# Kernel optimization log

Hardware: AMD Instinct MI355X
Metric: run time of the kernel (lower is better)

## Reference

```python
import jax, jax.numpy as jnp
import numpy as np

DECAY = 0.999
EPS = 1e-05
COMMIT = 0.25


def _layer_norm(x, g, b, eps=1e-5):
    mu = x.mean(-1, keepdims=True)
    var = ((x - mu) ** 2).mean(-1, keepdims=True)
    return (x - mu) * jax.lax.rsqrt(var + eps) * g + b


def setup_inputs() -> dict:
    key = jax.random.key(0)
    ks = jax.random.split(key, 8)
    B, T, D, M, H = 8, 4096, 512, 1024, 512
    init_bound = 1.0 / 512
    embedding = jax.random.uniform(ks[0], (M, D), jnp.float32, -init_bound, init_bound)
    return {
        "dense_x": jax.random.normal(ks[1], (B, T, D), jnp.float32),
        "dense_padding_mask": jax.random.randint(ks[2], (B, T), 0, 2).astype(bool),
        "labels": jax.random.randint(ks[3], (B, T), 0, M),
        "embedding": embedding,
        "ema_count": jnp.zeros((M,), jnp.float32),
        "ema_weight": embedding,
        "ln1_g": jnp.ones((D,), jnp.float32),
        "ln1_b": jnp.zeros((D,), jnp.float32),
        "W1": jax.random.normal(ks[4], (D, H), jnp.float32) * (1.0 / np.sqrt(D)),
        "ln2_g": jnp.ones((H,), jnp.float32),
        "ln2_b": jnp.zeros((H,), jnp.float32),
        "W2": jax.random.normal(ks[5], (H, M), jnp.float32) * (1.0 / np.sqrt(H)),
    }


def reference(dense_x, dense_padding_mask, labels, embedding, ema_count, ema_weight,
              ln1_g, ln1_b, W1, ln2_g, ln2_b, W2):
    B, T, D = dense_x.shape
    M = embedding.shape[0]
    N = B * T

    # ---- VQ codebook (EMA) ----
    x_flat = jax.lax.stop_gradient(dense_x).reshape(N, D)
    distances = (jnp.sum(embedding ** 2, axis=1)[None, :]
                 + jnp.sum(x_flat ** 2, axis=1, keepdims=True)
                 - 2.0 * (x_flat @ embedding.T))
    indices = jnp.argmin(distances, axis=-1)  # [N]
    quantized = embedding[indices].reshape(B, T, D)

    # EMA codebook update (training path); encodings.sum(0) and encodings.T @ x
    # expressed as scatter-adds instead of materializing [N, M] one-hot.
    counts = jnp.zeros((M,), dense_x.dtype).at[indices].add(1.0)
    new_count = DECAY * ema_count + (1.0 - DECAY) * counts
    n = jnp.sum(new_count)
    new_count = (new_count + EPS) / (n + M * EPS) * n
    dw = jnp.zeros((M, D), dense_x.dtype).at[indices].add(x_flat)
    new_weight = DECAY * ema_weight + (1.0 - DECAY) * dw
    new_embedding = new_weight / new_count[:, None]

    e_latent_loss = (dense_x - jax.lax.stop_gradient(quantized)) ** 2  # [B,T,D]
    vq_loss = COMMIT * e_latent_loss
    quantized_st = dense_x + jax.lax.stop_gradient(quantized - dense_x)

    avg_probs = counts / N
    perplexity = jnp.exp(-jnp.sum(avg_probs * jnp.log(avg_probs + 1e-10)))

    # ---- decoder: LN -> ReLU -> Linear -> LN -> ReLU -> Linear ----
    h = jax.nn.relu(_layer_norm(dense_x, ln1_g, ln1_b)) @ W1      # [B,T,H]
    logits = jax.nn.relu(_layer_norm(h, ln2_g, ln2_b)) @ W2       # [B,T,M]

    # ---- cross-entropy with ignore_index=-1 (padding) ----
    lab = jnp.where(dense_padding_mask, -1, labels)
    valid = lab >= 0
    safe = jnp.where(valid, lab, 0)
    logp = jax.nn.log_softmax(logits, axis=-1)
    ce = -jnp.take_along_axis(logp, safe[..., None], axis=-1)[..., 0]
    recon_loss = jnp.where(valid, ce, 0.0)

    loss = recon_loss + vq_loss.sum(-1)  # [B,T]
    return quantized_st, loss, perplexity, new_embedding, new_count, new_weight
```

## Files before the change

### kernel.cpp

```cpp
#include <hip/hip_runtime.h>


#define N_TOK 32768

typedef __attribute__((ext_vector_type(8))) short short8;
typedef __attribute__((ext_vector_type(4))) float f32x4;

__device__ __forceinline__ f32x4 mfma16(short8 a, short8 b, f32x4 c) {
    return __builtin_amdgcn_mfma_f32_16x16x32_bf16(a, b, c, 0, 0, 0);
}

__device__ __forceinline__ void gl_lds16(const void* g, void* l) {
    __builtin_amdgcn_global_load_lds(
        (const __attribute__((address_space(1))) void*)g,
        (__attribute__((address_space(3))) void*)l, 16, 0, 0);
}

__device__ __forceinline__ unsigned short f2bf(float x) {
    unsigned u = __float_as_uint(x);
    u += 0x7fffu + ((u >> 16) & 1u);
    return (unsigned short)(u >> 16);
}
__device__ __forceinline__ float bf2f(unsigned short h) {
    return __uint_as_float(((unsigned)h) << 16);
}

__device__ __forceinline__ float waveSum(float v) {
#pragma unroll
    for (int off = 32; off > 0; off >>= 1) v += __shfl_down(v, off, 64);
    return v;
}
__device__ __forceinline__ float xorSum(float v) {
#pragma unroll
    for (int off = 1; off < 64; off <<= 1) v += __shfl_xor(v, off);
    return v;
}

__device__ __forceinline__ void stage_tile128(const unsigned short* __restrict__ src,
                                              int r0, int k0, short* lds,
                                              int w, int lane) {
#pragma unroll
    for (int iss = 0; iss < 2; ++iss) {
        int L = (w << 11) + (iss << 10) + (lane << 4);
        int kb = L >> 11, m = (L >> 4) & 127;
        gl_lds16(src + (((size_t)(r0 + m)) << 9) + k0 + (kb << 3), (char*)lds + L);
    }
}

__global__ __launch_bounds__(256) void prep_x_kernel(
        const float* __restrict__ X, const float* __restrict__ g,
        const float* __restrict__ b, unsigned short* __restrict__ Xh,
        unsigned short* __restrict__ Xl, unsigned short* __restrict__ A1) {
    int lane = threadIdx.x & 63;
    int n = (blockIdx.x << 2) + (threadIdx.x >> 6);
    const float* row = X + ((size_t)n << 9);
    float v[8]; float s = 0.f, ss = 0.f;
#pragma unroll
    for (int i = 0; i < 8; ++i) { v[i] = row[lane + (i << 6)]; s += v[i]; ss += v[i] * v[i]; }
    s = xorSum(s); ss = xorSum(ss);
    float mu = s * (1.f / 512.f);
    float rs = rsqrtf(ss * (1.f / 512.f) - mu * mu + 1e-5f);
#pragma unroll
    for (int i = 0; i < 8; ++i) {
        int c = lane + (i << 6);
        size_t o = ((size_t)n << 9) + c;
        float x = v[i];
        unsigned short h = f2bf(x);
        Xh[o] = h;
        Xl[o] = f2bf(x - bf2f(h));
        float a = fmaxf((x - mu) * rs * g[c] + b[c], 0.f);
        A1[o] = f2bf(a);
    }
}

__global__ __launch_bounds__(256) void prep_h_kernel(
        const unsigned short* __restrict__ Hb, const float* __restrict__ g,
        const float* __restrict__ b, unsigned short* __restrict__ A2) {
    int lane = threadIdx.x & 63;
    int n = (blockIdx.x << 2) + (threadIdx.x >> 6);
    const unsigned short* row = Hb + ((size_t)n << 9);
    float v[8]; float s = 0.f, ss = 0.f;
#pragma unroll
    for (int i = 0; i < 8; ++i) { v[i] = bf2f(row[lane + (i << 6)]); s += v[i]; ss += v[i] * v[i]; }
    s = xorSum(s); ss = xorSum(ss);
    float mu = s * (1.f / 512.f);
    float rs = rsqrtf(ss * (1.f / 512.f) - mu * mu + 1e-5f);
#pragma unroll
    for (int i = 0; i < 8; ++i) {
        int c = lane + (i << 6);
        float a = fmaxf((v[i] - mu) * rs * g[c] + b[c], 0.f);
        A2[((size_t)n << 9) + c] = f2bf(a);
    }
}

__global__ __launch_bounds__(256) void prep_e_kernel(
        const float* __restrict__ E, unsigned short* __restrict__ Eh,
        unsigned short* __restrict__ El, float* __restrict__ e_sq) {
    int lane = threadIdx.x & 63;
    int m = (blockIdx.x << 2) + (threadIdx.x >> 6);
    const float* row = E + ((size_t)m << 9);
    float ss = 0.f;
#pragma unroll
    for (int i = 0; i < 8; ++i) {
        int c = lane + (i << 6);
        float x = row[c];
        ss += x * x;
        unsigned short h = f2bf(x);
        size_t o = ((size_t)m << 9) + c;
        Eh[o] = h;
        El[o] = f2bf(x - bf2f(h));
    }
    ss = xorSum(ss);
    if (lane == 0) e_sq[m] = ss;
}

__global__ __launch_bounds__(256) void prep_wt_kernel(
        const float* __restrict__ W, unsigned short* __restrict__ WT, int Nw) {
    __shared__ float t[32][33];
    int n0 = blockIdx.x << 5, k0 = blockIdx.y << 5;
    int tx = threadIdx.x & 31, ty = threadIdx.x >> 5;
#pragma unroll
    for (int l = 0; l < 4; ++l)
        t[ty + (l << 3)][tx] = W[(size_t)(k0 + ty + (l << 3)) * Nw + n0 + tx];
    __syncthreads();
#pragma unroll
    for (int l = 0; l < 4; ++l)
        WT[(((size_t)(n0 + ty + (l << 3))) << 9) + k0 + tx] = f2bf(t[tx][ty + (l << 3)]);
}

__device__ __forceinline__ unsigned long long packDist(float d, int m) {
    unsigned u = __float_as_uint(d);
    u = (u & 0x80000000u) ? ~u : (u | 0x80000000u);
    return ((unsigned long long)u << 32) | (unsigned)m;
}

__global__ __launch_bounds__(256) void dist_mfma_kernel(
        const unsigned short* __restrict__ Xh, const unsigned short* __restrict__ Xl,
        const unsigned short* __restrict__ Eh, const unsigned short* __restrict__ El,
        const float* __restrict__ e_sq, unsigned long long* __restrict__ minpack) {
    __shared__ __align__(16) short Ah[4096], Al[4096], Bh[4096], Bl[4096];
    int tid = threadIdx.x, lane = tid & 63, w = tid >> 6;
    int quad = lane >> 4, lanelo = lane & 15;
    int wm = w >> 1, wn = w & 1;
    int row0 = blockIdx.x << 7, m0 = blockIdx.y << 7;
    f32x4 acc[4][4];
#pragma unroll
    for (int i = 0; i < 4; ++i)
#pragma unroll
        for (int j = 0; j < 4; ++j) acc[i][j] = 0.f;

    for (int k0 = 0; k0 < 512; k0 += 32) {
        stage_tile128(Xh, row0, k0, Ah, w, lane);
        stage_tile128(Xl, row0, k0, Al, w, lane);
        stage_tile128(Eh, m0, k0, Bh, w, lane);
        stage_tile128(El, m0, k0, Bl, w, lane);
        __syncthreads();
        short8 ah[4], alr[4], bh[4], blr[4];
#pragma unroll
        for (int i = 0; i < 4; ++i) {
            int m = (wm << 6) + (i << 4) + lanelo;
            ah[i]  = *(const short8*)&Ah[(quad << 10) + (m << 3)];
            alr[i] = *(const short8*)&Al[(quad << 10) + (m << 3)];
        }
#pragma unroll
        for (int j = 0; j < 4; ++j) {
            int n = (wn << 6) + (j << 4) + lanelo;
            bh[j]  = *(const short8*)&Bh[(quad << 10) + (n << 3)];
            blr[j] = *(const short8*)&Bl[(quad << 10) + (n << 3)];
        }
#pragma unroll
        for (int i = 0; i < 4; ++i)
#pragma unroll
            for (int j = 0; j < 4; ++j) {
                acc[i][j] = mfma16(ah[i],  bh[j],  acc[i][j]);
                acc[i][j] = mfma16(alr[i], bh[j],  acc[i][j]);
                acc[i][j] = mfma16(ah[i],  blr[j], acc[i][j]);
            }
        __syncthreads();
    }

    float esq[4];
#pragma unroll
    for (int j = 0; j < 4; ++j) esq[j] = e_sq[m0 + (wn << 6) + (j << 4) + lanelo];
#pragma unroll
    for (int i = 0; i < 4; ++i)
#pragma unroll
        for (int r = 0; r < 4; ++r) {
            unsigned long long best = ~0ULL;
#pragma unroll
            for (int j = 0; j < 4; ++j) {
                int code = m0 + (wn << 6) + (j << 4) + lanelo;
                float d = esq[j] - 2.f * acc[i][j][r];
                unsigned long long p = packDist(d, code);
                if (p < best) best = p;
            }
#pragma unroll
            for (int off = 1; off < 16; off <<= 1) {
                unsigned long long q = __shfl_xor(best, off);
                if (q < best) best = q;
            }
            if (lanelo == 0) {
                int t = row0 + (wm << 6) + (i << 4) + (quad << 2) + r;
                atomicMin(&minpack[t], best);
            }
        }
}

__global__ __launch_bounds__(256) void gather_kernel(
        const float* __restrict__ X, const float* __restrict__ E,
        const unsigned long long* __restrict__ minpack,
        float* __restrict__ out_q, float* __restrict__ counts,
        float* __restrict__ vqsum) {
    int lane = threadIdx.x & 63;
    int n = (blockIdx.x << 2) + (threadIdx.x >> 6);
    int idx = (int)(minpack[n] & 0xFFFFFFFFULL);
    if (lane == 0) atomicAdd(&counts[idx], 1.0f);
    const float* xr = X + ((size_t)n << 9);
    const float* er = E + ((size_t)idx << 9);
    float s = 0.f;
#pragma unroll
    for (int i = 0; i < 8; ++i) {
        int c = lane + (i << 6);
        float xv = xr[c], q = er[c];
        out_q[((size_t)n << 9) + c] = q;
        float dlt = xv - q;
        s += dlt * dlt;
    }
    s = waveSum(s);
    if (lane == 0) vqsum[n] = 0.25f * s;
}

__global__ __launch_bounds__(256) void dw_kernel(
        const float* __restrict__ X, const unsigned long long* __restrict__ minpack,
        float* __restrict__ dw) {
    __shared__ float acc[4][512];
    int tid = threadIdx.x, lane = tid & 63, w = tid >> 6;
    int m = blockIdx.x;
    for (int c = lane; c < 512; c += 64) acc[w][c] = 0.f;
    for (int n0 = (w << 13); n0 < ((w + 1) << 13); n0 += 64) {
        int idx = (int)(minpack[n0 + lane] & 0xFFFFFFFFULL);
        unsigned long long hit = __ballot(idx == m);
        while (hit) {
            int t = __ffsll((unsigned long long)hit) - 1;
            hit &= hit - 1;
            const float* xr = X + ((size_t)(n0 + t) << 9);
#pragma unroll
            for (int i = 0; i < 8; ++i) acc[w][lane + (i << 6)] += xr[lane + (i << 6)];
        }
    }
    __syncthreads();
    for (int c = tid; c < 512; c += 256)
        dw[((size_t)m << 9) + c] = acc[0][c] + acc[1][c] + acc[2][c] + acc[3][c];
}

__global__ __launch_bounds__(256) void gemm1_mfma_kernel(
        const unsigned short* __restrict__ A1, const unsigned short* __restrict__ W1T,
        unsigned short* __restrict__ Hb) {
    __shared__ __align__(16) short As[4096], Bs[4096];
    int tid = threadIdx.x, lane = tid & 63, w = tid >> 6;
    int quad = lane >> 4, lanelo = lane & 15;
    int wm = w >> 1, wn = w & 1;
    int row0 = blockIdx.x << 7, n0 = blockIdx.y << 7;
    f32x4 acc[4][4];
#pragma unroll
    for (int i = 0; i < 4; ++i)
#pragma unroll
        for (int j = 0; j < 4; ++j) acc[i][j] = 0.f;

    for (int k0 = 0; k0 < 512; k0 += 32) {
        stage_tile128(A1, row0, k0, As, w, lane);
        stage_tile128(W1T, n0, k0, Bs, w, lane);
        __syncthreads();
        short8 af[4], bf[4];
#pragma unroll
        for (int i = 0; i < 4; ++i) {
            int m = (wm << 6) + (i << 4) + lanelo;
            af[i] = *(const short8*)&As[(quad << 10) + (m << 3)];
        }
#pragma unroll
        for (int j = 0; j < 4; ++j) {
            int n = (wn << 6) + (j << 4) + lanelo;
            bf[j] = *(const short8*)&Bs[(quad << 10) + (n << 3)];
        }
#pragma unroll
        for (int i = 0; i < 4; ++i)
#pragma unroll
            for (int j = 0; j < 4; ++j) acc[i][j] = mfma16(af[i], bf[j], acc[i][j]);
        __syncthreads();
    }
#pragma unroll
    for (int i = 0; i < 4; ++i)
#pragma unroll
        for (int j = 0; j < 4; ++j)
#pragma unroll
            for (int r = 0; r < 4; ++r) {
                int row = row0 + (wm << 6) + (i << 4) + (quad << 2) + r;
                int col = n0 + (wn << 6) + (j << 4) + lanelo;
                Hb[((size_t)row << 9) + col] = f2bf(acc[i][j][r]);
            }
}

__global__ __launch_bounds__(256) void gemm2_chunk_kernel(
        const unsigned short* __restrict__ A2, const unsigned short* __restrict__ W2T,
        const int* __restrict__ mask, const int* __restrict__ labels,
        float* __restrict__ ws_cmax, float* __restrict__ ws_csum,
        float* __restrict__ ws_lab) {
    __shared__ __align__(16) short As[4096], Bs[4096];
    __shared__ float lmax[2][2][64], lsum[2][2][64], llab[128];
    __shared__ int slab[128];
    int tid = threadIdx.x, lane = tid & 63, w = tid >> 6;
    int quad = lane >> 4, lanelo = lane & 15;
    int wm = w >> 1, wn = w & 1;
    int row0 = blockIdx.x << 7, c0 = blockIdx.y << 7;
    if (tid < 128) {
        int mk = mask[row0 + tid];
        slab[tid] = mk ? 0 : labels[row0 + tid];
    }
    f32x4 acc[4][4];
#pragma unroll
    for (int i = 0; i < 4; ++i)
#pragma unroll
        for (int j = 0; j < 4; ++j) acc[i][j] = 0.f;

    for (int k0 = 0; k0 < 512; k0 += 32) {
        stage_tile128(A2, row0, k0, As, w, lane);
        stage_tile128(W2T, c0, k0, Bs, w, lane);
        __syncthreads();
        short8 af[4], bf[4];
#pragma unroll
        for (int i = 0; i < 4; ++i) {
            int m = (wm << 6) + (i << 4) + lanelo;
            af[i] = *(const short8*)&As[(quad << 10) + (m << 3)];
        }
#pragma unroll
        for (int j = 0; j < 4; ++j) {
            int n = (wn << 6) + (j << 4) + lanelo;
            bf[j] = *(const short8*)&Bs[(quad << 10) + (n << 3)];
        }
#pragma unroll
        for (int i = 0; i < 4; ++i)
#pragma unroll
            for (int j = 0; j < 4; ++j) acc[i][j] = mfma16(af[i], bf[j], acc[i][j]);
        __syncthreads();
    }

#pragma unroll
    for (int i = 0; i < 4; ++i)
#pragma unroll
        for (int j = 0; j < 4; ++j)
#pragma unroll
            for (int r = 0; r < 4; ++r) {
                int code = c0 + (wn << 6) + (j << 4) + lanelo;
                int tt = (wm << 6) + (i << 4) + (quad << 2) + r;
                if (code == slab[tt]) llab[tt] = acc[i][j][r];
            }
#pragma unroll
    for (int i = 0; i < 4; ++i)
#pragma unroll
        for (int r = 0; r < 4; ++r) {
            float mx = fmaxf(fmaxf(acc[i][0][r], acc[i][1][r]),
                             fmaxf(acc[i][2][r], acc[i][3][r]));
#pragma unroll
            for (int off = 1; off < 16; off <<= 1) mx = fmaxf(mx, __shfl_xor(mx, off));
            if (lanelo == 0) lmax[wm][wn][(i << 4) + (quad << 2) + r] = mx;
        }
    __syncthreads();
#pragma unroll
    for (int i = 0; i < 4; ++i)
#pragma unroll
        for (int r = 0; r < 4; ++r) {
            int tl = (i << 4) + (quad << 2) + r;
            float cm = fmaxf(lmax[wm][0][tl], lmax[wm][1][tl]);
            float s = expf(acc[i][0][r] - cm) + expf(acc[i][1][r] - cm) +
                      expf(acc[i][2][r] - cm) + expf(acc[i][3][r] - cm);
#pragma unroll
            for (int off = 1; off < 16; off <<= 1) s += __shfl_xor(s, off);
            if (lanelo == 0) lsum[wm][wn][tl] = s;
        }
    __syncthreads();
    if (tid < 128) {
        int wmi = tid >> 6, tl = tid & 63;
        int token = row0 + tid;
        float cm = fmaxf(lmax[wmi][0][tl], lmax[wmi][1][tl]);
        float cs = lsum[wmi][0][tl] + lsum[wmi][1][tl];
        size_t o = ((size_t)blockIdx.y << 15) + token;
        ws_cmax[o] = cm;
        ws_csum[o] = cs;
        if ((slab[tid] >> 7) == (int)blockIdx.y) ws_lab[token] = llab[tid];
    }
}

__global__ __launch_bounds__(256) void ce_combine_kernel(
        const float* __restrict__ ws_cmax, const float* __restrict__ ws_csum,
        const float* __restrict__ ws_lab, const int* __restrict__ mask,
        const float* __restrict__ vqsum, float* __restrict__ loss_out) {
    int n = (blockIdx.x << 8) + threadIdx.x;
    float m[8], s[8];
#pragma unroll
    for (int c = 0; c < 8; ++c) {
        m[c] = ws_cmax[(c << 15) + n];
        s[c] = ws_csum[(c << 15) + n];
    }
    float gm = m[0];
#pragma unroll
    for (int c = 1; c < 8; ++c) gm = fmaxf(gm, m[c]);
    float se = 0.f;
#pragma unroll
    for (int c = 0; c < 8; ++c) se += s[c] * expf(m[c] - gm);
    float ce = -(ws_lab[n] - gm - logf(se));
    loss_out[n] = (mask[n] ? 0.f : ce) + vqsum[n];
}

__global__ __launch_bounds__(1024) void codebook_kernel(
        const float* __restrict__ ema_count, const float* __restrict__ counts,
        float* __restrict__ out_perp, float* __restrict__ out_newcount) {
    __shared__ float red[16];
    int tid = threadIdx.x;
    int lane = tid & 63, wid = tid >> 6;
    float cnt = counts[tid];
    float raw = 0.999f * ema_count[tid] + 0.001f * cnt;
    float v = waveSum(raw);
    if (lane == 0) red[wid] = v;
    __syncthreads();
    float nsum = 0.f;
#pragma unroll
    for (int i = 0; i < 16; ++i) nsum += red[i];
    __syncthreads();
    float p = cnt * (1.f / 32768.f);
    float e = p * logf(p + 1e-10f);
    e = waveSum(e);
    if (lane == 0) red[wid] = e;
    __syncthreads();
    float ent = 0.f;
#pragma unroll
    for (int i = 0; i < 16; ++i) ent += red[i];
    float nc = (raw + 1e-5f) / (nsum + 1024.f * 1e-5f) * nsum;
    out_newcount[tid] = nc;
    if (tid == 0) out_perp[0] = expf(-ent);
}

__global__ __launch_bounds__(256) void newweight_kernel(
        const float* __restrict__ ema_weight, const float* __restrict__ dw,
        const float* __restrict__ newcount, float* __restrict__ out_neww,
        float* __restrict__ out_newemb) {
    int i = (blockIdx.x << 8) + threadIdx.x;
    float nw = 0.999f * ema_weight[i] + 0.001f * dw[i];
    out_neww[i] = nw;
    out_newemb[i] = nw / newcount[i >> 9];
}

extern "C" void kernel_launch(void* const* d_in, const int* in_sizes, int n_in,
                              void* d_out, int out_size, void* d_ws, size_t ws_size,
                              hipStream_t stream) {
    const float* X          = (const float*)d_in[0];
    const int*   mask       = (const int*)d_in[1];
    const int*   labels     = (const int*)d_in[2];
    const float* E          = (const float*)d_in[3];
    const float* ema_count  = (const float*)d_in[4];
    const float* ema_weight = (const float*)d_in[5];
    const float* g1 = (const float*)d_in[6];
    const float* b1 = (const float*)d_in[7];
    const float* W1 = (const float*)d_in[8];
    const float* g2 = (const float*)d_in[9];
    const float* b2 = (const float*)d_in[10];
    const float* W2 = (const float*)d_in[11];

    float* out = (float*)d_out;
    float* out_q        = out;
    float* out_loss     = out + 16777216;
    float* out_perp     = out + 16809984;
    float* out_newemb   = out + 16809985;
    float* out_newcount = out + 17334273;
    float* out_neww     = out + 17335297;

    float* w = (float*)d_ws;
    float* vqsum = w;  w += 32768;
    float* e_sq = w;   w += 1024;
    float* counts = w; w += 1024;
    float* dwbuf = w;  w += 524288;
    unsigned long long* minpack = (unsigned long long*)w; w += 65536;
    float* ws_cmax = w; w += 262144;
    float* ws_csum = w; w += 262144;
    float* ws_lab  = w; w += 32768;
    unsigned short* Eh  = (unsigned short*)w; w += 262144;
    unsigned short* El  = (unsigned short*)w; w += 262144;
    unsigned short* W1T = (unsigned short*)w; w += 131072;
    unsigned short* W2T = (unsigned short*)w; w += 262144;
    unsigned short* Xh  = (unsigned short*)w; w += 8388608;
    unsigned short* Xl  = (unsigned short*)w; w += 8388608;
    unsigned short* A1  = (unsigned short*)w; w += 8388608;
    unsigned short* A2  = Xh;
    unsigned short* Hb  = Xl;

    hipMemsetAsync(counts, 0, 1024 * sizeof(float), stream);
    hipMemsetAsync(minpack, 0xFF, (size_t)N_TOK * sizeof(unsigned long long), stream);

    prep_e_kernel<<<256, 256, 0, stream>>>(E, Eh, El, e_sq);
    prep_wt_kernel<<<dim3(16, 16), 256, 0, stream>>>(W1, W1T, 512);
    prep_wt_kernel<<<dim3(32, 16), 256, 0, stream>>>(W2, W2T, 1024);
    prep_x_kernel<<<8192, 256, 0, stream>>>(X, g1, b1, Xh, Xl, A1);
    dist_mfma_kernel<<<dim3(256, 8), 256, 0, stream>>>(Xh, Xl, Eh, El, e_sq, minpack);
    gather_kernel<<<8192, 256, 0, stream>>>(X, E, minpack, out_q, counts, vqsum);
    dw_kernel<<<1024, 256, 0, stream>>>(X, minpack, dwbuf);
    gemm1_mfma_kernel<<<dim3(256, 4), 256, 0, stream>>>(A1, W1T, Hb);
    prep_h_kernel<<<8192, 256, 0, stream>>>(Hb, g2, b2, A2);
    gemm2_chunk_kernel<<<dim3(256, 8), 256, 0, stream>>>(A2, W2T, mask, labels,
                                                         ws_cmax, ws_csum, ws_lab);
    ce_combine_kernel<<<128, 256, 0, stream>>>(ws_cmax, ws_csum, ws_lab,
                                               mask, vqsum, out_loss);
    codebook_kernel<<<1, 1024, 0, stream>>>(ema_count, counts, out_perp, out_newcount);
    newweight_kernel<<<2048, 256, 0, stream>>>(ema_weight, dwbuf, out_newcount,
                                               out_neww, out_newemb);
}
```

Measured before the change: 548.5 us.

## Use fp16 two-term distance GEMM and bucket tokens by code for dw

The VQ distance GEMM drops from three bf16 MFMAs per tile (split X and split E) to two fp16 MFMAs. X is stored as a single fp16 value and the codebook is pre-scaled by 512 and split into fp16 hi/lo parts, which also removes one LDS staging buffer and one global input stream. The dw accumulation no longer has each of 1024 blocks scan all 32768 indices with ballots. Instead, integer counts feed a prefix-sum in the codebook kernel, a scatter kernel builds per-code token buckets, and dw reads only its own bucket. This adds two small kernels and an extra 16 MB workspace buffer for Hb, and a single fp16 copy of X may change argmin tie-breaking near equal distances.

```diff
diff --git a/kernel.cpp b/kernel.cpp
--- a/kernel.cpp
+++ b/kernel.cpp
@@ -4,10 +4,14 @@
 #define N_TOK 32768
 
 typedef __attribute__((ext_vector_type(8))) short short8;
+typedef _Float16 half8 __attribute__((ext_vector_type(8)));
 typedef __attribute__((ext_vector_type(4))) float f32x4;
 
 __device__ __forceinline__ f32x4 mfma16(short8 a, short8 b, f32x4 c) {
     return __builtin_amdgcn_mfma_f32_16x16x32_bf16(a, b, c, 0, 0, 0);
+}
+__device__ __forceinline__ f32x4 mfma16h(half8 a, half8 b, f32x4 c) {
+    return __builtin_amdgcn_mfma_f32_16x16x32_f16(a, b, c, 0, 0, 0);
 }
 
 __device__ __forceinline__ void gl_lds16(const void* g, void* l) {
@@ -24,6 +28,16 @@
 __device__ __forceinline__ float bf2f(unsigned short h) {
     return __uint_as_float(((unsigned)h) << 16);
 }
+__device__ __forceinline__ unsigned short f2h(float x) {
+    union { _Float16 h; unsigned short u; } c;
+    c.h = (_Float16)x;
+    return c.u;
+}
+__device__ __forceinline__ float h2f(unsigned short u) {
+    union { _Float16 h; unsigned short u; } c;
+    c.u = u;
+    return (float)c.h;
+}
 
 __device__ __forceinline__ float waveSum(float v) {
 #pragma unroll
@@ -49,8 +63,8 @@
 
 __global__ __launch_bounds__(256) void prep_x_kernel(
         const float* __restrict__ X, const float* __restrict__ g,
-        const float* __restrict__ b, unsigned short* __restrict__ Xh,
-        unsigned short* __restrict__ Xl, unsigned short* __restrict__ A1) {
+        const float* __restrict__ b, unsigned short* __restrict__ Xf,
+        unsigned short* __restrict__ A1) {
     int lane = threadIdx.x & 63;
     int n = (blockIdx.x << 2) + (threadIdx.x >> 6);
     const float* row = X + ((size_t)n << 9);
@@ -65,9 +79,7 @@
         int c = lane + (i << 6);
         size_t o = ((size_t)n << 9) + c;
         float x = v[i];
-        unsigned short h = f2bf(x);
-        Xh[o] = h;
-        Xl[o] = f2bf(x - bf2f(h));
+        Xf[o] = f2h(x);
         float a = fmaxf((x - mu) * rs * g[c] + b[c], 0.f);
         A1[o] = f2bf(a);
     }
@@ -94,8 +106,8 @@
 }
 
 __global__ __launch_bounds__(256) void prep_e_kernel(
-        const float* __restrict__ E, unsigned short* __restrict__ Eh,
-        unsigned short* __restrict__ El, float* __restrict__ e_sq) {
+        const float* __restrict__ E, unsigned short* __restrict__ Ehf,
+        unsigned short* __restrict__ Elf, float* __restrict__ e_sq) {
     int lane = threadIdx.x & 63;
     int m = (blockIdx.x << 2) + (threadIdx.x >> 6);
     const float* row = E + ((size_t)m << 9);
@@ -105,13 +117,14 @@
         int c = lane + (i << 6);
         float x = row[c];
         ss += x * x;
-        unsigned short h = f2bf(x);
+        float xs = x * 512.f;
+        unsigned short h = f2h(xs);
         size_t o = ((size_t)m << 9) + c;
-        Eh[o] = h;
-        El[o] = f2bf(x - bf2f(h));
+        Ehf[o] = h;
+        Elf[o] = f2h(xs - h2f(h));
     }
     ss = xorSum(ss);
-    if (lane == 0) e_sq[m] = ss;
+    if (lane == 0) e_sq[m] = ss * 512.f;
 }
 
 __global__ __launch_bounds__(256) void prep_wt_kernel(
@@ -135,10 +148,10 @@
 }
 
 __global__ __launch_bounds__(256) void dist_mfma_kernel(
-        const unsigned short* __restrict__ Xh, const unsigned short* __restrict__ Xl,
-        const unsigned short* __restrict__ Eh, const unsigned short* __restrict__ El,
+        const unsigned short* __restrict__ Xf,
+        const unsigned short* __restrict__ Ehf, const unsigned short* __restrict__ Elf,
         const float* __restrict__ e_sq, unsigned long long* __restrict__ minpack) {
-    __shared__ __align__(16) short Ah[4096], Al[4096], Bh[4096], Bl[4096];
+    __shared__ __align__(16) short Axs[4096], Bh[4096], Bl[4096];
     int tid = threadIdx.x, lane = tid & 63, w = tid >> 6;
     int quad = lane >> 4, lanelo = lane & 15;
     int wm = w >> 1, wn = w & 1;
@@ -150,31 +163,28 @@
         for (int j = 0; j < 4; ++j) acc[i][j] = 0.f;
 
     for (int k0 = 0; k0 < 512; k0 += 32) {
-        stage_tile128(Xh, row0, k0, Ah, w, lane);
-        stage_tile128(Xl, row0, k0, Al, w, lane);
-        stage_tile128(Eh, m0, k0, Bh, w, lane);
-        stage_tile128(El, m0, k0, Bl, w, lane);
-        __syncthreads();
-        short8 ah[4], alr[4], bh[4], blr[4];
+        stage_tile128(Xf, row0, k0, Axs, w, lane);
+        stage_tile128(Ehf, m0, k0, Bh, w, lane);
+        stage_tile128(Elf, m0, k0, Bl, w, lane);
+        __syncthreads();
+        half8 av[4], bh[4], bl[4];
 #pragma unroll
         for (int i = 0; i < 4; ++i) {
             int m = (wm << 6) + (i << 4) + lanelo;
-            ah[i]  = *(const short8*)&Ah[(quad << 10) + (m << 3)];
-            alr[i] = *(const short8*)&Al[(quad << 10) + (m << 3)];
+            av[i] = __builtin_bit_cast(half8, *(const short8*)&Axs[(quad << 10) + (m << 3)]);
         }
 #pragma unroll
         for (int j = 0; j < 4; ++j) {
             int n = (wn << 6) + (j << 4) + lanelo;
-            bh[j]  = *(const short8*)&Bh[(quad << 10) + (n << 3)];
-            blr[j] = *(const short8*)&Bl[(quad << 10) + (n << 3)];
+            bh[j] = __builtin_bit_cast(half8, *(const short8*)&Bh[(quad << 10) + (n << 3)]);
+            bl[j] = __builtin_bit_cast(half8, *(const short8*)&Bl[(quad << 10) + (n << 3)]);
         }
 #pragma unroll
         for (int i = 0; i < 4; ++i)
 #pragma unroll
             for (int j = 0; j < 4; ++j) {
-                acc[i][j] = mfma16(ah[i],  bh[j],  acc[i][j]);
-                acc[i][j] = mfma16(alr[i], bh[j],  acc[i][j]);
-                acc[i][j] = mfma16(ah[i],  blr[j], acc[i][j]);
+                acc[i][j] = mfma16h(av[i], bh[j], acc[i][j]);
+                acc[i][j] = mfma16h(av[i], bl[j], acc[i][j]);
             }
         __syncthreads();
     }
@@ -209,12 +219,12 @@
 __global__ __launch_bounds__(256) void gather_kernel(
         const float* __restrict__ X, const float* __restrict__ E,
         const unsigned long long* __restrict__ minpack,
-        float* __restrict__ out_q, float* __restrict__ counts,
+        float* __restrict__ out_q, int* __restrict__ icounts,
         float* __restrict__ vqsum) {
     int lane = threadIdx.x & 63;
     int n = (blockIdx.x << 2) + (threadIdx.x >> 6);
     int idx = (int)(minpack[n] & 0xFFFFFFFFULL);
-    if (lane == 0) atomicAdd(&counts[idx], 1.0f);
+    if (lane == 0) atomicAdd(&icounts[idx], 1);
     const float* xr = X + ((size_t)n << 9);
     const float* er = E + ((size_t)idx << 9);
     float s = 0.f;
@@ -230,27 +240,77 @@
     if (lane == 0) vqsum[n] = 0.25f * s;
 }
 
+__global__ __launch_bounds__(1024) void codebook_kernel(
+        const float* __restrict__ ema_count, const int* __restrict__ icounts,
+        float* __restrict__ out_perp, float* __restrict__ out_newcount,
+        int* __restrict__ offsets) {
+    __shared__ int sc[1024];
+    __shared__ float red[16];
+    int tid = threadIdx.x;
+    int lane = tid & 63, wid = tid >> 6;
+    int ic = icounts[tid];
+    sc[tid] = ic;
+    for (int off = 1; off < 1024; off <<= 1) {
+        __syncthreads();
+        int v = (tid >= off) ? sc[tid - off] : 0;
+        __syncthreads();
+        sc[tid] += v;
+    }
+    offsets[tid] = sc[tid] - ic;
+    __syncthreads();
+
+    float cnt = (float)ic;
+    float raw = 0.999f * ema_count[tid] + 0.001f * cnt;
+    float v = waveSum(raw);
+    if (lane == 0) red[wid] = v;
+    __syncthreads();
+    float nsum = 0.f;
+#pragma unroll
+    for (int i = 0; i < 16; ++i) nsum += red[i];
+    __syncthreads();
+    float p = cnt * (1.f / 32768.f);
+    float e = p * logf(p + 1e-10f);
+    e = waveSum(e);
+    if (lane == 0) red[wid] = e;
+    __syncthreads();
+    float ent = 0.f;
+#pragma unroll
+    for (int i = 0; i < 16; ++i) ent += red[i];
+    float nc = (raw + 1e-5f) / (nsum + 1024.f * 1e-5f) * nsum;
+    out_newcount[tid] = nc;
+    if (tid == 0) out_perp[0] = expf(-ent);
+}
+
+__global__ __launch_bounds__(256) void scatter_kernel(
+        const unsigned long long* __restrict__ minpack,
+        const int* __restrict__ offsets, int* __restrict__ cursor,
+        int* __restrict__ bucket) {
+    int n = (blockIdx.x << 8) + threadIdx.x;
+    int idx = (int)(minpack[n] & 0xFFFFFFFFULL);
+    int pos = atomicAdd(&cursor[idx], 1);
+    bucket[offsets[idx] + pos] = n;
+}
+
 __global__ __launch_bounds__(256) void dw_kernel(
-        const float* __restrict__ X, const unsigned long long* __restrict__ minpack,
+        const float* __restrict__ X, const int* __restrict__ bucket,
+        const int* __restrict__ icounts, const int* __restrict__ offsets,
         float* __restrict__ dw) {
-    __shared__ float acc[4][512];
+    __shared__ float comb[4][512];
     int tid = threadIdx.x, lane = tid & 63, w = tid >> 6;
     int m = blockIdx.x;
-    for (int c = lane; c < 512; c += 64) acc[w][c] = 0.f;
-    for (int n0 = (w << 13); n0 < ((w + 1) << 13); n0 += 64) {
-        int idx = (int)(minpack[n0 + lane] & 0xFFFFFFFFULL);
-        unsigned long long hit = __ballot(idx == m);
-        while (hit) {
-            int t = __ffsll((unsigned long long)hit) - 1;
-            hit &= hit - 1;
-            const float* xr = X + ((size_t)(n0 + t) << 9);
-#pragma unroll
-            for (int i = 0; i < 8; ++i) acc[w][lane + (i << 6)] += xr[lane + (i << 6)];
-        }
-    }
+    int cnt = icounts[m], base = offsets[m];
+    float acc[8] = {};
+    for (int i = w; i < cnt; i += 4) {
+        int t = bucket[base + i];
+        const float* xr = X + ((size_t)t << 9);
+#pragma unroll
+        for (int j = 0; j < 8; ++j) acc[j] += xr[lane + (j << 6)];
+    }
+#pragma unroll
+    for (int j = 0; j < 8; ++j) comb[w][lane + (j << 6)] = acc[j];
     __syncthreads();
     for (int c = tid; c < 512; c += 256)
-        dw[((size_t)m << 9) + c] = acc[0][c] + acc[1][c] + acc[2][c] + acc[3][c];
+        dw[((size_t)m << 9) + c] = comb[0][c] + comb[1][c] + comb[2][c] + comb[3][c];
 }
 
 __global__ __launch_bounds__(256) void gemm1_mfma_kernel(
@@ -411,34 +471,6 @@
     loss_out[n] = (mask[n] ? 0.f : ce) + vqsum[n];
 }
 
-__global__ __launch_bounds__(1024) void codebook_kernel(
-        const float* __restrict__ ema_count, const float* __restrict__ counts,
-        float* __restrict__ out_perp, float* __restrict__ out_newcount) {
-    __shared__ float red[16];
-    int tid = threadIdx.x;
-    int lane = tid & 63, wid = tid >> 6;
-    float cnt = counts[tid];
-    float raw = 0.999f * ema_count[tid] + 0.001f * cnt;
-    float v = waveSum(raw);
-    if (lane == 0) red[wid] = v;
-    __syncthreads();
-    float nsum = 0.f;
-#pragma unroll
-    for (int i = 0; i < 16; ++i) nsum += red[i];
-    __syncthreads();
-    float p = cnt * (1.f / 32768.f);
-    float e = p * logf(p + 1e-10f);
-    e = waveSum(e);
-    if (lane == 0) red[wid] = e;
-    __syncthreads();
-    float ent = 0.f;
-#pragma unroll
-    for (int i = 0; i < 16; ++i) ent += red[i];
-    float nc = (raw + 1e-5f) / (nsum + 1024.f * 1e-5f) * nsum;
-    out_newcount[tid] = nc;
-    if (tid == 0) out_perp[0] = expf(-ent);
-}
-
 __global__ __launch_bounds__(256) void newweight_kernel(
         const float* __restrict__ ema_weight, const float* __restrict__ dw,
         const float* __restrict__ newcount, float* __restrict__ out_neww,
@@ -476,39 +508,43 @@
     float* w = (float*)d_ws;
     float* vqsum = w;  w += 32768;
     float* e_sq = w;   w += 1024;
-    float* counts = w; w += 1024;
     float* dwbuf = w;  w += 524288;
     unsigned long long* minpack = (unsigned long long*)w; w += 65536;
     float* ws_cmax = w; w += 262144;
     float* ws_csum = w; w += 262144;
     float* ws_lab  = w; w += 32768;
-    unsigned short* Eh  = (unsigned short*)w; w += 262144;
-    unsigned short* El  = (unsigned short*)w; w += 262144;
+    int* icounts = (int*)w; w += 1024;
+    int* cursor  = (int*)w; w += 1024;
+    int* offsets = (int*)w; w += 1024;
+    int* bucket  = (int*)w; w += 32768;
+    unsigned short* Ehf = (unsigned short*)w; w += 262144;
+    unsigned short* Elf = (unsigned short*)w; w += 262144;
     unsigned short* W1T = (unsigned short*)w; w += 131072;
     unsigned short* W2T = (unsigned short*)w; w += 262144;
-    unsigned short* Xh  = (unsigned short*)w; w += 8388608;
-    unsigned short* Xl  = (unsigned short*)w; w += 8388608;
+    unsigned short* Xf  = (unsigned short*)w; w += 8388608;
     unsigned short* A1  = (unsigned short*)w; w += 8388608;
-    unsigned short* A2  = Xh;
-    unsigned short* Hb  = Xl;
-
-    hipMemsetAsync(counts, 0, 1024 * sizeof(float), stream);
+    unsigned short* Hb  = (unsigned short*)w; w += 8388608;
+    unsigned short* A2  = Xf;
+
+    hipMemsetAsync(icounts, 0, 2048 * sizeof(int), stream);
     hipMemsetAsync(minpack, 0xFF, (size_t)N_TOK * sizeof(unsigned long long), stream);
 
-    prep_e_kernel<<<256, 256, 0, stream>>>(E, Eh, El, e_sq);
+    prep_e_kernel<<<256, 256, 0, stream>>>(E, Ehf, Elf, e_sq);
     prep_wt_kernel<<<dim3(16, 16), 256, 0, stream>>>(W1, W1T, 512);
     prep_wt_kernel<<<dim3(32, 16), 256, 0, stream>>>(W2, W2T, 1024);
-    prep_x_kernel<<<8192, 256, 0, stream>>>(X, g1, b1, Xh, Xl, A1);
-    dist_mfma_kernel<<<dim3(256, 8), 256, 0, stream>>>(Xh, Xl, Eh, El, e_sq, minpack);
-    gather_kernel<<<8192, 256, 0, stream>>>(X, E, minpack, out_q, counts, vqsum);
-    dw_kernel<<<1024, 256, 0, stream>>>(X, minpack, dwbuf);
+    prep_x_kernel<<<8192, 256, 0, stream>>>(X, g1, b1, Xf, A1);
+    dist_mfma_kernel<<<dim3(256, 8), 256, 0, stream>>>(Xf, Ehf, Elf, e_sq, minpack);
+    gather_kernel<<<8192, 256, 0, stream>>>(X, E, minpack, out_q, icounts, vqsum);
+    codebook_kernel<<<1, 1024, 0, stream>>>(ema_count, icounts, out_perp,
+                                            out_newcount, offsets);
+    scatter_kernel<<<128, 256, 0, stream>>>(minpack, offsets, cursor, bucket);
+    dw_kernel<<<1024, 256, 0, stream>>>(X, bucket, icounts, offsets, dwbuf);
     gemm1_mfma_kernel<<<dim3(256, 4), 256, 0, stream>>>(A1, W1T, Hb);
     prep_h_kernel<<<8192, 256, 0, stream>>>(Hb, g2, b2, A2);
     gemm2_chunk_kernel<<<dim3(256, 8), 256, 0, stream>>>(A2, W2T, mask, labels,
                                                          ws_cmax, ws_csum, ws_lab);
     ce_combine_kernel<<<128, 256, 0, stream>>>(ws_cmax, ws_csum, ws_lab,
                                                mask, vqsum, out_loss);
-    codebook_kernel<<<1, 1024, 0, stream>>>(ema_count, counts, out_perp, out_newcount);
     newweight_kernel<<<2048, 256, 0, stream>>>(ema_weight, dwbuf, out_newcount,
                                                out_neww, out_newemb);
 }
```

After: 491.0 us. -10.5%, faster.
